# Performance work log

Measured on AMD Instinct MI355X. Metric: run time of the kernel, lower is better.

Reference implementation:

```python
import jax, jax.numpy as jnp
import numpy as np
import math

B, L, S, E, D = 32, 2048, 2048, 64, 64

def setup_inputs() -> dict:
    key = jax.random.key(0)
    kq, kk, kv = jax.random.split(key, 3)
    return {
        "queries": jax.random.normal(kq, (B, L, E), dtype=jnp.float32),
        "keys":    jax.random.normal(kk, (B, S, E), dtype=jnp.float32),
        "values":  jax.random.normal(kv, (B, S, D), dtype=jnp.float32),
    }

def reference(queries, keys, values):
    # scale = 1/sqrt(E) since self.scale is None
    scale = 1.0 / math.sqrt(queries.shape[-1])
    # unfused QK^T -> softmax -> V (dropout is identity at inference)
    scores = jnp.einsum('ble,bse->bls', queries, keys)  # [B,L,S]
    # mask_flag branch not taken because L == S (matches torch code path)
    A = jax.nn.softmax(scale * scores, axis=-1)
    V = jnp.einsum('bls,bsd->bld', A, values)  # [B,L,D]
    return V
```

## Files before the change

### kernel.cpp

```cpp
#include <hip/hip_runtime.h>
#include <hip/hip_bf16.h>


#define B_ 32
#define L_ 2048
#define S_ 2048
#define E_ 64
#define D_ 64
#define BQ 128
#define NIMG 32
#define IMG_BYTES 16384
#define NCHUNK 16

typedef __attribute__((ext_vector_type(8))) short bf16x8;
typedef __attribute__((ext_vector_type(16))) float f32x16;
typedef __attribute__((ext_vector_type(4))) unsigned u32x4;

__device__ __forceinline__ unsigned short f2b(float f) {
  unsigned u = __builtin_bit_cast(unsigned, f);
  u += 0x7fff + ((u >> 16) & 1);
  return (unsigned short)(u >> 16);
}

__device__ __forceinline__ unsigned pk2(float a, float b) {
#if defined(__has_builtin) && __has_builtin(__builtin_amdgcn_cvt_pk_bf16_f32)
  typedef __bf16 b2 __attribute__((ext_vector_type(2)));
  b2 t = __builtin_amdgcn_cvt_pk_bf16_f32(a, b);
  return __builtin_bit_cast(unsigned, t);
#else
  return (unsigned)f2b(a) | ((unsigned)f2b(b) << 16);
#endif
}

__device__ __forceinline__ float fexp2(float x) {
#if defined(__has_builtin) && __has_builtin(__builtin_amdgcn_exp2f)
  return __builtin_amdgcn_exp2f(x);
#else
  return exp2f(x);
#endif
}

__device__ __forceinline__ void cp16(const void* g, void* lbase) {
#if defined(__has_builtin) && __has_builtin(__builtin_amdgcn_global_load_lds)
  typedef const __attribute__((address_space(1))) void gvoid;
  typedef __attribute__((address_space(3))) void lvoid;
  __builtin_amdgcn_global_load_lds((gvoid*)g, (lvoid*)lbase, 16, 0, 0);
#endif
}

__global__ __launch_bounds__(256) void prepass(
    const float* __restrict__ K, const float* __restrict__ V,
    char* __restrict__ ws) {
  __shared__ __align__(16) short vimg[4096];

  const int tid  = threadIdx.x;
  const int lane = tid & 63;
  const int quad = lane >> 4;
  const int qb0  = quad & 1;
  const int qb1  = (quad >> 1) & 1;

  const int b  = blockIdx.x >> 5;
  const int c  = blockIdx.x & 31;
  const int s0 = c * 64;

  const float* Kb = K + (long)b * S_ * E_;
  const float* Vb = V + (long)b * S_ * D_;
  short* img = (short*)(ws + (size_t)blockIdx.x * IMG_BYTES);

#pragma unroll
  for (int it = 0; it < 4; ++it) {
    const int i  = tid + it * 256;
    const int s  = i >> 4;
    const int c4 = (i & 15) << 2;

    float4 kv = *(const float4*)(Kb + (long)(s0 + s) * E_ + c4);
    {
      int g = (c4 >> 3) ^ (s & 7);
      *(uint2*)&img[s * 64 + g * 8 + (c4 & 7)] = make_uint2(pk2(kv.x, kv.y), pk2(kv.z, kv.w));
    }

    float4 vv = *(const float4*)(Vb + (long)(s0 + s) * D_ + c4);
    float a0 = vv.x, a1 = vv.y, a2 = vv.z, a3 = vv.w;
    float s0f = qb1 ? a0 : a2;
    float s1f = qb1 ? a1 : a3;
    float r0  = __shfl_xor(s0f, 32);
    float r1  = __shfl_xor(s1f, 32);
    float b0 = qb1 ? r0 : a0;
    float b1 = qb1 ? r1 : a1;
    float b2 = qb1 ? a2 : r0;
    float b3 = qb1 ? a3 : r1;
    float t0 = qb0 ? b0 : b1;
    float t1 = qb0 ? b2 : b3;
    float u0 = __shfl_xor(t0, 16);
    float u1 = __shfl_xor(t1, 16);
    float w0 = qb0 ? u0 : b0;
    float w1 = qb0 ? b1 : u0;
    float w2 = qb0 ? u1 : b2;
    float w3 = qb0 ? b3 : u1;
    const int base = s - quad;
    const int d    = c4 + quad;
    int g = (base >> 3) ^ (d & 7);
    *(uint2*)&vimg[d * 64 + g * 8 + (base & 7)] = make_uint2(pk2(w0, w1), pk2(w2, w3));
  }

  __syncthreads();

  {
    const char* src = (const char*)vimg + tid * 32;
    char* dst = (char*)img + 8192 + tid * 32;
    *(float4*)(dst)      = *(const float4*)(src);
    *(float4*)(dst + 16) = *(const float4*)(src + 16);
  }
}

__global__ __launch_bounds__(512, 4) void attn_fwd(
    const float* __restrict__ Q, const char* __restrict__ ws,
    float* __restrict__ O) {
  __shared__ __align__(16) char smem[65536 + 1024];
  float* Obuf = (float*)smem;
  float* ML   = (float*)(smem + 65536);

  const int tid  = threadIdx.x;
  const int lane = tid & 63;
  const int wv   = tid >> 6;
  const int l31  = lane & 31;
  const int h    = lane >> 5;
  const int qg   = wv >> 1;
  const int kh   = wv & 1;
  const int sb   = qg & 1;

  const int i_ = blockIdx.x;
  const int x_ = i_ & 7;
  const int j_ = i_ >> 3;
  const int b  = (x_ << 2) | (j_ >> 4);
  const int q0 = (j_ & 15) * BQ;

  const float SCALE2 = 0.125f * 1.44269504088896340736f;
  const char* img0 = ws + (size_t)b * ((size_t)NIMG * IMG_BYTES);

#pragma unroll
  for (int j = 0; j < 4; ++j)
    cp16(img0 + wv * 4096 + j * 1024 + lane * 16, smem + wv * 4096 + j * 1024);

  bf16x8 qf[4];
  {
    const float* qrow = Q + ((long)b * L_ + q0 + qg * 32 + l31) * E_;
#pragma unroll
    for (int ke = 0; ke < 4; ++ke) {
      const float* sp = qrow + ke * 16 + h * 8;
      float4 x = *(const float4*)(sp);
      float4 y = *(const float4*)(sp + 4);
      u32x4 uu = { pk2(x.x * SCALE2, x.y * SCALE2), pk2(x.z * SCALE2, x.w * SCALE2),
                   pk2(y.x * SCALE2, y.y * SCALE2), pk2(y.z * SCALE2, y.w * SCALE2) };
      qf[ke] = __builtin_bit_cast(bf16x8, uu);
    }
  }

  int pl = l31;
  {
    const int blk = (pl >> 2) & 3;
    if (blk == 1) pl += 4;
    else if (blk == 2) pl -= 4;
  }

  const int kb = (kh * 16384 + (pl << 7) + ((h ^ (pl & 7)) << 4)) ^ (sb << 12);
  const int vb = (kh * 16384 + 8192 + (l31 << 7) + ((h ^ (l31 & 7)) << 4)) ^ (sb << 6);

  f32x16 o[2];
#pragma unroll
  for (int mt = 0; mt < 2; ++mt)
#pragma unroll
    for (int r = 0; r < 16; ++r) o[mt][r] = 0.f;
  float lrun = 0.f;

  __syncthreads();

#define CHUNK_BODY(TT, BUFB, OTHB)                                             \
  {                                                                            \
    if ((TT) + 1 < NCHUNK) {                                                   \
      const char* img = img0 + (size_t)((TT) + 1) * 32768;                     \
      _Pragma("unroll")                                                        \
      for (int j = 0; j < 4; ++j)                                              \
        cp16(img + wv * 4096 + j * 1024 + lane * 16,                           \
             smem + (OTHB) + wv * 4096 + j * 1024);                            \
    }                                                                          \
    _Pragma("unroll")                                                          \
    for (int nt = 0; nt < 2; ++nt) {                                           \
      bf16x8 kf[4];                                                            \
      _Pragma("unroll")                                                        \
      for (int ke = 0; ke < 4; ++ke)                                           \
        kf[ke] = *(const bf16x8*)(smem +                                       \
                   (kb ^ ((BUFB) | (nt << 12) | (ke << 5))));                  \
      f32x16 acc;                                                              \
      _Pragma("unroll")                                                        \
      for (int r = 0; r < 16; ++r) acc[r] = 0.f;                               \
      __builtin_amdgcn_s_setprio(1);                                           \
      _Pragma("unroll")                                                        \
      for (int ke = 0; ke < 4; ++ke)                                           \
        acc = __builtin_amdgcn_mfma_f32_32x32x16_bf16(kf[ke], qf[ke], acc,     \
                                                      0, 0, 0);                \
      __builtin_amdgcn_s_setprio(0);                                           \
      u32x4 f0, f1;                                                            \
      _Pragma("unroll")                                                        \
      for (int gixx = 0; gixx < 4; ++gixx) {                                   \
        float p0 = fexp2(acc[2 * gixx]);                                       \
        float p1 = fexp2(acc[2 * gixx + 1]);                                   \
        float p2 = fexp2(acc[8 + 2 * gixx]);                                   \
        float p3 = fexp2(acc[8 + 2 * gixx + 1]);                               \
        f0[gixx] = pk2(p0, p1);                                                \
        f1[gixx] = pk2(p2, p3);                                                \
        lrun += (p0 + p1) + (p2 + p3);                                         \
      }                                                                        \
      bf16x8 pf0 = __builtin_bit_cast(bf16x8, f0);                             \
      bf16x8 pf1 = __builtin_bit_cast(bf16x8, f1);                             \
      __builtin_amdgcn_s_setprio(1);                                           \
      _Pragma("unroll")                                                        \
      for (int mt = 0; mt < 2; ++mt) {                                         \
        bf16x8 vf0 = *(const bf16x8*)(smem +                                   \
                      (vb ^ ((BUFB) | (mt << 12) | ((nt * 2 + 0) << 5))));     \
        o[mt] = __builtin_amdgcn_mfma_f32_32x32x16_bf16(vf0, pf0, o[mt],       \
                                                        0, 0, 0);              \
        bf16x8 vf1 = *(const bf16x8*)(smem +                                   \
                      (vb ^ ((BUFB) | (mt << 12) | ((nt * 2 + 1) << 5))));     \
        o[mt] = __builtin_amdgcn_mfma_f32_32x32x16_bf16(vf1, pf1, o[mt],       \
                                                        0, 0, 0);              \
      }                                                                        \
      __builtin_amdgcn_s_setprio(0);                                           \
    }                                                                          \
    __syncthreads();                                                           \
  }

  for (int t = 0; t < NCHUNK; t += 2) {
    CHUNK_BODY(t, 0, 32768)
    CHUNK_BODY(t + 1, 32768, 0)
  }
#undef CHUNK_BODY

  float lt = lrun + __shfl_xor(lrun, 32);

  if (lane < 32)
    ML[(qg * 2 + kh) * 32 + l31] = lt;
  __syncthreads();

  const float inv = 1.f / (lt + ML[(qg * 2 + (kh ^ 1)) * 32 + l31]);
  const int q = qg * 32 + l31;

  if (kh == 1) {
#pragma unroll
    for (int mt = 0; mt < 2; ++mt)
#pragma unroll
      for (int r = 0; r < 16; ++r) {
        const int d = mt * 32 + (r & 3) + 8 * (r >> 2) + 4 * h;
        Obuf[q * 68 + d] = o[mt][r];
      }
  }
  __syncthreads();

  if (kh == 0) {
#pragma unroll
    for (int mt = 0; mt < 2; ++mt)
#pragma unroll
      for (int r = 0; r < 16; ++r) {
        const int d = mt * 32 + (r & 3) + 8 * (r >> 2) + 4 * h;
        Obuf[q * 68 + d] = (o[mt][r] + Obuf[q * 68 + d]) * inv;
      }
  }
  __syncthreads();

  {
    const int qq = tid >> 2;
    const int dh = (tid & 3) * 16;
    float* orow = O + ((long)b * L_ + q0 + qq) * D_ + dh;
    const float* src = &Obuf[qq * 68 + dh];
#pragma unroll
    for (int j = 0; j < 4; ++j)
      *(float4*)(orow + j * 4) = *(const float4*)(src + j * 4);
  }
}

extern "C" void kernel_launch(void* const* d_in, const int* in_sizes, int n_in,
                              void* d_out, int out_size, void* d_ws, size_t ws_size,
                              hipStream_t stream) {
  const float* Q = (const float*)d_in[0];
  const float* K = (const float*)d_in[1];
  const float* V = (const float*)d_in[2];
  float* O = (float*)d_out;

  prepass<<<dim3(B_ * NIMG), dim3(256), 0, stream>>>(K, V, (char*)d_ws);
  attn_fwd<<<dim3(B_ * (L_ / BQ)), dim3(512), 0, stream>>>(Q, (const char*)d_ws, O);
}
```

Measured before the change: 140.7 us.

## Load V fragments directly from global in MFMA layout, stage only K in LDS

The preprocessing kernel now writes V into the workspace in the exact per-lane MFMA fragment order, so the attention kernel can load V operands straight from global memory (L2-resident) instead of staging them through shared memory. Only K is double-buffered in LDS now, which shrinks shared memory from about 66KB to 35KB per block and halves the async copy traffic into LDS. This may raise achievable occupancy and cut LDS bandwidth pressure, but it adds global-load latency inside the inner loop that must be hidden by the prefetch distance within each iteration.

Measured after the change: 147.8 us. 5.1% more time.

```diff
diff --git a/kernel.cpp b/kernel.cpp
--- a/kernel.cpp
+++ b/kernel.cpp
@@ -106,19 +106,30 @@
   __syncthreads();
 
   {
-    const char* src = (const char*)vimg + tid * 32;
-    char* dst = (char*)img + 8192 + tid * 32;
-    *(float4*)(dst)      = *(const float4*)(src);
-    *(float4*)(dst + 16) = *(const float4*)(src + 16);
+    const int tau = tid >> 5;
+    const int u2  = (tid & 31) << 1;
+    const int mt  = tau >> 2;
+    const int s16 = tau & 3;
+#pragma unroll
+    for (int lam = 0; lam < 2; ++lam) {
+      const int l    = u2 + lam;
+      const int hh   = l >> 5;
+      const int l31v = l & 31;
+      const int d    = mt * 32 + l31v;
+      const int oct  = s16 * 2 + hh;
+      const int g    = oct ^ (d & 7);
+      const float4 frag = *(const float4*)&vimg[d * 64 + g * 8];
+      *(float4*)((char*)img + 8192 + tau * 1024 + l * 16) = frag;
+    }
   }
 }
 
 __global__ __launch_bounds__(512, 4) void attn_fwd(
     const float* __restrict__ Q, const char* __restrict__ ws,
     float* __restrict__ O) {
-  __shared__ __align__(16) char smem[65536 + 1024];
+  __shared__ __align__(16) char smem[35840];
   float* Obuf = (float*)smem;
-  float* ML   = (float*)(smem + 65536);
+  float* ML   = (float*)(smem + 34816);
 
   const int tid  = threadIdx.x;
   const int lane = tid & 63;
@@ -127,7 +138,6 @@
   const int h    = lane >> 5;
   const int qg   = wv >> 1;
   const int kh   = wv & 1;
-  const int sb   = qg & 1;
 
   const int i_ = blockIdx.x;
   const int x_ = i_ & 7;
@@ -139,8 +149,11 @@
   const char* img0 = ws + (size_t)b * ((size_t)NIMG * IMG_BYTES);
 
 #pragma unroll
-  for (int j = 0; j < 4; ++j)
-    cp16(img0 + wv * 4096 + j * 1024 + lane * 16, smem + wv * 4096 + j * 1024);
+  for (int j = 0; j < 2; ++j)
+    cp16(img0 + (wv >> 2) * 16384 + (wv & 3) * 2048 + j * 1024 + lane * 16,
+         smem + wv * 2048 + j * 1024);
+
+  const char* vgb = img0 + kh * 16384 + 8192 + 4096 + lane * 16;
 
   bf16x8 qf[4];
   {
@@ -163,8 +176,7 @@
     else if (blk == 2) pl -= 4;
   }
 
-  const int kb = (kh * 16384 + (pl << 7) + ((h ^ (pl & 7)) << 4)) ^ (sb << 12);
-  const int vb = (kh * 16384 + 8192 + (l31 << 7) + ((h ^ (l31 & 7)) << 4)) ^ (sb << 6);
+  const int kb = kh * 8192 + (pl << 7) + ((h ^ (pl & 7)) << 4);
 
   f32x16 o[2];
 #pragma unroll
@@ -178,14 +190,20 @@
 #define CHUNK_BODY(TT, BUFB, OTHB)                                             \
   {                                                                            \
     if ((TT) + 1 < NCHUNK) {                                                   \
-      const char* img = img0 + (size_t)((TT) + 1) * 32768;                     \
-      _Pragma("unroll")                                                        \
-      for (int j = 0; j < 4; ++j)                                              \
-        cp16(img + wv * 4096 + j * 1024 + lane * 16,                           \
-             smem + (OTHB) + wv * 4096 + j * 1024);                            \
+      const char* img = img0 + (size_t)(2 * ((TT) + 1) + (wv >> 2)) * 16384;   \
+      _Pragma("unroll")                                                        \
+      for (int j = 0; j < 2; ++j)                                              \
+        cp16(img + (wv & 3) * 2048 + j * 1024 + lane * 16,                     \
+             smem + (OTHB) + wv * 2048 + j * 1024);                            \
     }                                                                          \
+    const char* vp = vgb + (size_t)(TT) * 32768;                               \
     _Pragma("unroll")                                                          \
     for (int nt = 0; nt < 2; ++nt) {                                           \
+          \
+      bf16x8 v00 = *(const bf16x8*)(vp + (((nt * 2 + 0) << 10) - 4096));       \
+      bf16x8 v01 = *(const bf16x8*)(vp + (((nt * 2 + 1) << 10) - 4096));       \
+      bf16x8 v10 = *(const bf16x8*)(vp + (((4 + nt * 2 + 0) << 10) - 4096));   \
+      bf16x8 v11 = *(const bf16x8*)(vp + (((4 + nt * 2 + 1) << 10) - 4096));   \
       bf16x8 kf[4];                                                            \
       _Pragma("unroll")                                                        \
       for (int ke = 0; ke < 4; ++ke)                                           \
@@ -214,25 +232,18 @@
       bf16x8 pf0 = __builtin_bit_cast(bf16x8, f0);                             \
       bf16x8 pf1 = __builtin_bit_cast(bf16x8, f1);                             \
       __builtin_amdgcn_s_setprio(1);                                           \
-      _Pragma("unroll")                                                        \
-      for (int mt = 0; mt < 2; ++mt) {                                         \
-        bf16x8 vf0 = *(const bf16x8*)(smem +                                   \
-                      (vb ^ ((BUFB) | (mt << 12) | ((nt * 2 + 0) << 5))));     \
-        o[mt] = __builtin_amdgcn_mfma_f32_32x32x16_bf16(vf0, pf0, o[mt],       \
-                                                        0, 0, 0);              \
-        bf16x8 vf1 = *(const bf16x8*)(smem +                                   \
-                      (vb ^ ((BUFB) | (mt << 12) | ((nt * 2 + 1) << 5))));     \
-        o[mt] = __builtin_amdgcn_mfma_f32_32x32x16_bf16(vf1, pf1, o[mt],       \
-                                                        0, 0, 0);              \
-      }                                                                        \
+      o[0] = __builtin_amdgcn_mfma_f32_32x32x16_bf16(v00, pf0, o[0], 0, 0, 0); \
+      o[1] = __builtin_amdgcn_mfma_f32_32x32x16_bf16(v10, pf0, o[1], 0, 0, 0); \
+      o[0] = __builtin_amdgcn_mfma_f32_32x32x16_bf16(v01, pf1, o[0], 0, 0, 0); \
+      o[1] = __builtin_amdgcn_mfma_f32_32x32x16_bf16(v11, pf1, o[1], 0, 0, 0); \
       __builtin_amdgcn_s_setprio(0);                                           \
     }                                                                          \
     __syncthreads();                                                           \
   }
 
   for (int t = 0; t < NCHUNK; t += 2) {
-    CHUNK_BODY(t, 0, 32768)
-    CHUNK_BODY(t + 1, 32768, 0)
+    CHUNK_BODY(t, 0, 16384)
+    CHUNK_BODY(t + 1, 16384, 0)
   }
 #undef CHUNK_BODY
 
```
